# Kernel optimization log

Hardware: AMD Instinct MI355X
Metric: run time of the kernel (lower is better)

Reference implementation:

```python
import jax, jax.numpy as jnp
from jax import lax
import numpy as np

# int24 / PrecisionSplit constants (all exactly representable in float32)
TWO12 = 4096.0      # 2**12
TWO13 = 8192.0      # 2**13
TWO23 = 8388608.0   # 2**23
TWO24 = 16777216.0  # 2**24
TWO25 = 33554432.0  # 2**25

N_ITER = 64
N_CHANNELS = 256
BATCH = 4096


def _wrap(v, half, full):
    # two's-complement wrap of integer-valued floats to signed range [-half, half)
    return jnp.mod(v + half, full) - half


def _cast_up_i24(v):
    # GMACv2(int24, [1]) on a single input: round to integer grid and wrap to int24
    return _wrap(jnp.round(v), TWO23, TWO24)


def setup_inputs() -> dict:
    key = jax.random.key(0)
    k1, _ = jax.random.split(key)
    # scale so values exercise a wide chunk of the int24 range after rounding
    x = jax.random.normal(k1, (BATCH, N_ITER * N_CHANNELS), dtype=jnp.float32) * 1.0e5
    s_init = jnp.zeros((N_CHANNELS,), dtype=jnp.float32)
    return {"x": x, "s_init": s_init}


def reference(x, s_init):
    B = x.shape[0]
    n_ch = s_init.shape[0]
    n_iter = x.shape[-1] // n_ch

    # cast_up1 / cast_up2: quantize inputs to int24
    x_i = _cast_up_i24(x)            # [B, n_iter*n_ch]
    s0 = _cast_up_i24(s_init)        # [n_ch]
    s0 = jnp.broadcast_to(s0, (B, n_ch))

    # i24SumLoop: sequential GMAC accumulate with int24 wrapping per step.
    # Per-step partial sums stay within |v| < 2**24 so float32 stays exact.
    xs = x_i.reshape(B, n_iter, n_ch).transpose(1, 0, 2)  # [n_iter, B, n_ch]

    def step(carry, xi):
        s = _wrap(carry + xi, TWO23, TWO24)
        return s, None

    y, _ = lax.scan(step, s0, xs)    # [B, n_ch], int24-wrapped

    # PrecisionSplit([12, 13], [16, 16]): split (up to 25-bit) value into
    # low 12 bits (unsigned) and high 13 bits (signed), each held in 16-bit words.
    y_u = jnp.mod(y, TWO25)                             # unsigned 25-bit view
    y_lo = jnp.mod(y_u, TWO12)                          # low 12 bits
    y_hi = _wrap(jnp.floor(y_u / TWO12), TWO12, TWO13)  # high 13 bits, signed
    return (y_lo, y_hi)
```

## Files before the change

kernel.cpp:

```cpp
#include <hip/hip_runtime.h>
#include <cstdint>

#define N_ITER 64
#define N_CH 256
#define BATCH 4096
#define OUT_PLANE (BATCH * N_CH)

typedef float v4f __attribute__((ext_vector_type(4)));
typedef int   v4i __attribute__((ext_vector_type(4)));
typedef float v2f __attribute__((ext_vector_type(2)));

__device__ __forceinline__ v2f split_ref_fp32(int y) {
    uint32_t u;
    if (y >= 0) {
        u = (uint32_t)y;
    } else {
        u = (uint32_t)(y + 33554432);
        int m = y & 3;
        if (m == 1)      u -= 1u;
        else if (m == 3) u += 1u;
    }
    v2f r;
    r.x = (float)(u & 0xFFFu);
    int q = (int)(u >> 12);
    r.y = (float)(((q + 4096) & 8191) - 4096);
    return r;
}

__global__ __launch_bounds__(256) void i24sum_kernel(const float* __restrict__ x,
                                                     const float* __restrict__ s_init,
                                                     float* __restrict__ out) {
    const int tid  = threadIdx.x;
    const int lane = tid & 63;
    const int wave = tid >> 6;
    const int row  = blockIdx.x;

    const v4f* xr = reinterpret_cast<const v4f*>(x) + (size_t)row * (N_ITER * N_CH / 4);

    v4i acc = (v4i)0;
#pragma unroll
    for (int k = 0; k < 16; ++k) {
        const int i = (wave << 4) + k;
        v4f v = __builtin_nontemporal_load(xr + i * (N_CH / 4) + lane);
        acc.x += (int)rintf(v.x);
        acc.y += (int)rintf(v.y);
        acc.z += (int)rintf(v.z);
        acc.w += (int)rintf(v.w);
    }

    __shared__ v4i part[4][64];
    part[wave][lane] = acc;
    __syncthreads();

    if (wave == 0) {
        const v4f s4 = reinterpret_cast<const v4f*>(s_init)[lane];
        v4i t = part[0][lane];
        t += part[1][lane];
        t += part[2][lane];
        t += part[3][lane];
        t.x += (int)rintf(s4.x);
        t.y += (int)rintf(s4.y);
        t.z += (int)rintf(s4.z);
        t.w += (int)rintf(s4.w);

        t.x = (t.x << 8) >> 8;
        t.y = (t.y << 8) >> 8;
        t.z = (t.z << 8) >> 8;
        t.w = (t.w << 8) >> 8;

        const v2f sx = split_ref_fp32(t.x);
        const v2f sy = split_ref_fp32(t.y);
        const v2f sz = split_ref_fp32(t.z);
        const v2f sw = split_ref_fp32(t.w);

        v4f lo4, hi4;
        lo4.x = sx.x; hi4.x = sx.y;
        lo4.y = sy.x; hi4.y = sy.y;
        lo4.z = sz.x; hi4.z = sz.y;
        lo4.w = sw.x; hi4.w = sw.y;

        const int ovec = row * (N_CH / 4) + lane;
        reinterpret_cast<v4f*>(out)[ovec] = lo4;
        reinterpret_cast<v4f*>(out + OUT_PLANE)[ovec] = hi4;
    }
}

extern "C" void kernel_launch(void* const* d_in, const int* in_sizes, int n_in,
                              void* d_out, int out_size, void* d_ws, size_t ws_size,
                              hipStream_t stream) {
    const float* x      = (const float*)d_in[0];
    const float* s_init = (const float*)d_in[1];
    float*       out    = (float*)d_out;

    dim3 grid(BATCH);
    dim3 block(256);
    i24sum_kernel<<<grid, block, 0, stream>>>(x, s_init, out);
}
```

Measured before the change: 335.3 us.

## Split reduction into partial-sum kernel and separate split kernel via workspace

Each wave now reduces half of a row's 64 iterations (32 loads in chunks of 8), and partial sums go to a global workspace instead of shared memory. A second kernel adds the two partials, applies the int24 wrap and precision split, and writes the outputs. This removes the block barrier and the idle waves during the final stage, at the cost of a second launch and an extra workspace write and read.

```diff
diff --git a/kernel.cpp b/kernel.cpp
--- a/kernel.cpp
+++ b/kernel.cpp
@@ -27,62 +27,71 @@
     return r;
 }
 
-__global__ __launch_bounds__(256) void i24sum_kernel(const float* __restrict__ x,
-                                                     const float* __restrict__ s_init,
-                                                     float* __restrict__ out) {
+__global__ __launch_bounds__(256) void i24_partial_kernel(const float* __restrict__ x,
+                                                          int* __restrict__ ws) {
     const int tid  = threadIdx.x;
     const int lane = tid & 63;
     const int wave = tid >> 6;
-    const int row  = blockIdx.x;
+    const int W    = blockIdx.x * 4 + wave;
+    const int row  = W >> 1;
+    const int half = W & 1;
 
-    const v4f* xr = reinterpret_cast<const v4f*>(x) + (size_t)row * (N_ITER * N_CH / 4);
+    const v4f* xr = reinterpret_cast<const v4f*>(x)
+                  + (size_t)row * (N_ITER * N_CH / 4)
+                  + (size_t)half * (32 * N_CH / 4);
 
     v4i acc = (v4i)0;
+    for (int j = 0; j < 4; ++j) {
 #pragma unroll
-    for (int k = 0; k < 16; ++k) {
-        const int i = (wave << 4) + k;
-        v4f v = __builtin_nontemporal_load(xr + i * (N_CH / 4) + lane);
-        acc.x += (int)rintf(v.x);
-        acc.y += (int)rintf(v.y);
-        acc.z += (int)rintf(v.z);
-        acc.w += (int)rintf(v.w);
+        for (int k = 0; k < 8; ++k) {
+            v4f v = __builtin_nontemporal_load(xr + (j * 8 + k) * (N_CH / 4) + lane);
+            acc.x += (int)rintf(v.x);
+            acc.y += (int)rintf(v.y);
+            acc.z += (int)rintf(v.z);
+            acc.w += (int)rintf(v.w);
+        }
     }
 
-    __shared__ v4i part[4][64];
-    part[wave][lane] = acc;
-    __syncthreads();
+    reinterpret_cast<v4i*>(ws)[(size_t)W * 64 + lane] = acc;
+}
 
-    if (wave == 0) {
-        const v4f s4 = reinterpret_cast<const v4f*>(s_init)[lane];
-        v4i t = part[0][lane];
-        t += part[1][lane];
-        t += part[2][lane];
-        t += part[3][lane];
-        t.x += (int)rintf(s4.x);
-        t.y += (int)rintf(s4.y);
-        t.z += (int)rintf(s4.z);
-        t.w += (int)rintf(s4.w);
+__global__ __launch_bounds__(256) void i24_split_kernel(const int* __restrict__ ws,
+                                                        const float* __restrict__ s_init,
+                                                        float* __restrict__ out) {
+    const int tid  = threadIdx.x;
+    const int lane = tid & 63;
+    const int wave = tid >> 6;
+    const int row  = blockIdx.x * 4 + wave;
 
-        t.x = (t.x << 8) >> 8;
-        t.y = (t.y << 8) >> 8;
-        t.z = (t.z << 8) >> 8;
-        t.w = (t.w << 8) >> 8;
+    const v4i* p = reinterpret_cast<const v4i*>(ws) + (size_t)row * 128;
+    v4i t = p[lane];
+    t += p[64 + lane];
 
-        const v2f sx = split_ref_fp32(t.x);
-        const v2f sy = split_ref_fp32(t.y);
-        const v2f sz = split_ref_fp32(t.z);
-        const v2f sw = split_ref_fp32(t.w);
+    const v4f s4 = reinterpret_cast<const v4f*>(s_init)[lane];
+    t.x += (int)rintf(s4.x);
+    t.y += (int)rintf(s4.y);
+    t.z += (int)rintf(s4.z);
+    t.w += (int)rintf(s4.w);
 
-        v4f lo4, hi4;
-        lo4.x = sx.x; hi4.x = sx.y;
-        lo4.y = sy.x; hi4.y = sy.y;
-        lo4.z = sz.x; hi4.z = sz.y;
-        lo4.w = sw.x; hi4.w = sw.y;
+    t.x = (t.x << 8) >> 8;
+    t.y = (t.y << 8) >> 8;
+    t.z = (t.z << 8) >> 8;
+    t.w = (t.w << 8) >> 8;
 
-        const int ovec = row * (N_CH / 4) + lane;
-        reinterpret_cast<v4f*>(out)[ovec] = lo4;
-        reinterpret_cast<v4f*>(out + OUT_PLANE)[ovec] = hi4;
-    }
+    const v2f sx = split_ref_fp32(t.x);
+    const v2f sy = split_ref_fp32(t.y);
+    const v2f sz = split_ref_fp32(t.z);
+    const v2f sw = split_ref_fp32(t.w);
+
+    v4f lo4, hi4;
+    lo4.x = sx.x; hi4.x = sx.y;
+    lo4.y = sy.x; hi4.y = sy.y;
+    lo4.z = sz.x; hi4.z = sz.y;
+    lo4.w = sw.x; hi4.w = sw.y;
+
+    const int ovec = row * (N_CH / 4) + lane;
+    reinterpret_cast<v4f*>(out)[ovec] = lo4;
+    reinterpret_cast<v4f*>(out + OUT_PLANE)[ovec] = hi4;
 }
 
 extern "C" void kernel_launch(void* const* d_in, const int* in_sizes, int n_in,
@@ -91,8 +100,8 @@
     const float* x      = (const float*)d_in[0];
     const float* s_init = (const float*)d_in[1];
     float*       out    = (float*)d_out;
+    int*         ws     = (int*)d_ws;
 
-    dim3 grid(BATCH);
-    dim3 block(256);
-    i24sum_kernel<<<grid, block, 0, stream>>>(x, s_init, out);
+    i24_partial_kernel<<<dim3(2048), dim3(256), 0, stream>>>(x, ws);
+    i24_split_kernel<<<dim3(1024), dim3(256), 0, stream>>>(ws, s_init, out);
 }
```

New measurement: 337.9 us. No clear change (+0.8%).
